# Performance work log

Measured on AMD Instinct MI355X. Metric: run time of the kernel, lower is better.

Reference implementation:

```python
import jax, jax.numpy as jnp
import numpy as np


def _mlp(x, W1, b1, W2, b2):
    # x: (B, M, T); torch MLPLayer: transpose(1,2) -> Linear -> Linear -> LeakyReLU -> transpose back
    h = jnp.einsum('bmt,hm->bht', x, W1) + b1[None, :, None]   # (B, H, T)
    y = jnp.einsum('bht,oh->bot', h, W2) + b2[None, :, None]   # (B, M, T)
    return jax.nn.leaky_relu(y, negative_slope=0.01)


def _calc_attn(q, k, v):
    # q: (B, M, Tq), k: (B, M, Tk), v: (B, M, Tk)
    Tq = q.shape[-1]
    qk = jnp.einsum('bmq,bmk->bqk', q, k)                       # (B, Tq, Tk)
    eye = jnp.eye(Tq, dtype=qk.dtype)                           # broadcasts: (Tq,Tq) or (1,1)
    logits = jnp.exp(qk - qk * eye / jnp.sqrt(jnp.asarray(Tq, qk.dtype)))
    scores = jax.nn.softmax(logits, axis=-1)
    return jnp.einsum('bqk,bmk->bmq', scores, v)                # (B, M, Tq)


def setup_inputs() -> dict:
    key = jax.random.key(0)
    B, M, T, H = 16, 128, 2048, 512
    ks = jax.random.split(key, 14)
    s = 0.02
    inp = {
        'pattern': jax.random.normal(ks[0], (B, M, T), jnp.float32),
        'value': jax.random.normal(ks[1], (B, M, T), jnp.float32),
        'kernel_size': 33,
    }
    names = ['q', 'k', 'o']
    for i, n in enumerate(names):
        inp['W%s1' % n] = jax.random.normal(ks[2 + 4 * i], (H, M), jnp.float32) * s
        inp['b%s1' % n] = jax.random.normal(ks[3 + 4 * i], (H,), jnp.float32) * s
        inp['W%s2' % n] = jax.random.normal(ks[4 + 4 * i], (M, H), jnp.float32) * s
        inp['b%s2' % n] = jax.random.normal(ks[5 + 4 * i], (M,), jnp.float32) * s
    return inp


def reference(pattern, value, kernel_size, Wq1, bq1, Wq2, bq2, Wk1, bk1, Wk2, bk2, Wo1, bo1, Wo2, bo2):
    query = _mlp(pattern, Wq1, bq1, Wq2, bq2)
    key = _mlp(pattern, Wk1, bk1, Wk2, bk2)
    # full (internal) attention
    attn_in = _calc_attn(query, key, value)                     # (B, M, T)
    rep_in = _mlp(attn_in, Wo1, bo1, Wo2, bo2)
    # windowed (external) attention
    T = query.shape[-1]
    cu = (kernel_size - 1) // 2
    q_w = query[..., T - 1 - cu : T - cu]                       # (B, M, 1)
    k_w = key[..., kernel_size - cu - 1 : T - cu - 2]           # (B, M, T-k-1)
    v_w = value[..., kernel_size : T - 1]                       # (B, M, T-k-1)
    attn_ex = _calc_attn(q_w, k_w, v_w)                         # (B, M, 1)
    rep_ex = _mlp(attn_ex, Wo1, bo1, Wo2, bo2)
    return jnp.concatenate([rep_in, rep_ex], axis=-1)           # (B, M, T+1)
```

## Files before the change

### kernel.cpp

```cpp
#include <hip/hip_runtime.h>
#include <hip/hip_bf16.h>
#include <math.h>

#define B_    16
#define M_    128
#define T_    2048
#define H_    512
#define TOUT_ 2049

typedef unsigned short u16;
typedef unsigned int   u32;
typedef __bf16 bf16x8 __attribute__((ext_vector_type(8)));
typedef float  f32x16 __attribute__((ext_vector_type(16)));
typedef float  f32x4  __attribute__((ext_vector_type(4)));
typedef u32    u32x4  __attribute__((ext_vector_type(4)));
typedef u32    u32x2  __attribute__((ext_vector_type(2)));

#define A_OFF     0
#define C_OFF     16384
#define MEAN_OFF  16896
#define AQKBF_OFF 19200
#define AOBF_OFF  35584
#define QT_OFF    43776
#define KT_OFF    (43776 + 2097152)
#define VB_OFF    (43776 + 2 * 2097152)

static __device__ __forceinline__ u16 f2bf(float f) {
  u32 u = __float_as_uint(f);
  u = (u + 0x7FFFu + ((u >> 16) & 1u)) >> 16;
  return (u16)u;
}
static __device__ __forceinline__ u32 pk2(float lo, float hi) {
  __hip_bfloat162 h = __float22bfloat162_rn(float2{lo, hi});
  u32 r;
  __builtin_memcpy(&r, &h, 4);
  return r;
}
static __device__ __forceinline__ bf16x8 ldfrag(const u16* p) {
  return __builtin_bit_cast(bf16x8, *(const u32x4*)p);
}

__global__ __launch_bounds__(128) void fuse_weights_all(
    const float* __restrict__ W1q, const float* __restrict__ b1q,
    const float* __restrict__ W2q, const float* __restrict__ b2q,
    const float* __restrict__ W1k, const float* __restrict__ b1k,
    const float* __restrict__ W2k, const float* __restrict__ b2k,
    const float* __restrict__ W1o, const float* __restrict__ b1o,
    const float* __restrict__ W2o, const float* __restrict__ b2o,
    float* __restrict__ A, float* __restrict__ c,
    u16* __restrict__ Aqk_bf, u16* __restrict__ Ao_bf) {
  __shared__ float w2row[H_];
  int which = blockIdx.x >> 7;
  int o = blockIdx.x & 127;
  const float* W1 = which == 0 ? W1q : which == 1 ? W1k : W1o;
  const float* b1 = which == 0 ? b1q : which == 1 ? b1k : b1o;
  const float* W2 = which == 0 ? W2q : which == 1 ? W2k : W2o;
  const float* b2 = which == 0 ? b2q : which == 1 ? b2k : b2o;
  int m = threadIdx.x;
  for (int h = m; h < H_; h += 128) w2row[h] = W2[o * H_ + h];
  __syncthreads();
  float acc = 0.f;
#pragma unroll 8
  for (int h = 0; h < H_; ++h) acc = fmaf(w2row[h], W1[h * M_ + m], acc);
  u16 ab = f2bf(acc);
  if (which == 0)      Aqk_bf[o * 128 + m] = ab;
  else if (which == 1) Aqk_bf[(128 + o) * 128 + m] = ab;
  else               { Ao_bf[o * 128 + m] = ab; A[o * M_ + m] = acc; }
  if (m < 64) {
    float cc = 0.f;
    for (int h = m; h < H_; h += 64) cc = fmaf(w2row[h], b1[h], cc);
#pragma unroll
    for (int off = 32; off > 0; off >>= 1) cc += __shfl_down(cc, off, 64);
    if (m == 0) c[which * 128 + o] = cc + b2[o];
  }
}

#define XS 68

__global__ __launch_bounds__(256) void prep_kernel(
    const float* __restrict__ pattern, const u16* __restrict__ Aqk_bf,
    const float* __restrict__ cqk, u16* __restrict__ qT, u16* __restrict__ kT,
    const float* __restrict__ value, u16* __restrict__ vb,
    float* __restrict__ meanv) {
  __shared__ alignas(16) float xsf[128 * XS];
  int bx = blockIdx.x;
  int tid = threadIdx.x;

  if (bx >= 512) {
    int bm = bx - 512;
    float* red = xsf;
    const float* row = value + (size_t)bm * T_;
    int i0 = tid * 8;
    float4 a = *(const float4*)(row + i0);
    float4 bq = *(const float4*)(row + i0 + 4);
    u32x4 o = {pk2(a.x, a.y), pk2(a.z, a.w), pk2(bq.x, bq.y), pk2(bq.z, bq.w)};
    *(u32x4*)&vb[(size_t)bm * T_ + i0] = o;
    float vals[8] = {a.x, a.y, a.z, a.w, bq.x, bq.y, bq.z, bq.w};
    float s = 0.f;
#pragma unroll
    for (int j = 0; j < 8; ++j) {
      int idx = i0 + j;
      if (idx >= 33 && idx < T_ - 1) s += vals[j];
    }
    red[tid] = s;
    __syncthreads();
    for (int st = 128; st > 0; st >>= 1) {
      if (tid < st) red[tid] += red[tid + st];
      __syncthreads();
    }
    if (tid == 0) meanv[bm] = red[0] * (1.f / 2014.f);
    return;
  }

  int b = bx >> 5;
  int t0 = (bx & 31) * 64;
  int lane = tid & 63;
  int wv = tid >> 6;
  int l31 = lane & 31;
  int lh8 = (lane >> 5) * 8;

  bf16x8 afr[2][8];
#pragma unroll
  for (int i = 0; i < 2; ++i) {
    const u16* ap = Aqk_bf + ((2 * wv + i) * 32 + l31) * 128 + lh8;
#pragma unroll
    for (int s = 0; s < 8; ++s) afr[i][s] = ldfrag(ap + 16 * s);
  }

#pragma unroll
  for (int rep = 0; rep < 8; ++rep) {
    int m = rep * 16 + (tid >> 4);
    int tc = (tid & 15) * 4;
    float4 v = *(const float4*)&pattern[(size_t)(b * M_ + m) * T_ + t0 + tc];
    *(float4*)&xsf[m * XS + tc] = v;
  }
  __syncthreads();

  bf16x8 bfr[2][8];
#pragma unroll
  for (int tt = 0; tt < 2; ++tt) {
#pragma unroll
    for (int s = 0; s < 8; ++s) {
      float v0 = xsf[(s * 16 + lh8 + 0) * XS + tt * 32 + l31];
      float v1 = xsf[(s * 16 + lh8 + 1) * XS + tt * 32 + l31];
      float v2 = xsf[(s * 16 + lh8 + 2) * XS + tt * 32 + l31];
      float v3 = xsf[(s * 16 + lh8 + 3) * XS + tt * 32 + l31];
      float v4 = xsf[(s * 16 + lh8 + 4) * XS + tt * 32 + l31];
      float v5 = xsf[(s * 16 + lh8 + 5) * XS + tt * 32 + l31];
      float v6 = xsf[(s * 16 + lh8 + 6) * XS + tt * 32 + l31];
      float v7 = xsf[(s * 16 + lh8 + 7) * XS + tt * 32 + l31];
      u32x4 p = {pk2(v0, v1), pk2(v2, v3), pk2(v4, v5), pk2(v6, v7)};
      bfr[tt][s] = __builtin_bit_cast(bf16x8, p);
    }
  }
  __syncthreads();

  u16* obuf = (u16*)xsf;
#pragma unroll
  for (int tt = 0; tt < 2; ++tt) {
#pragma unroll
    for (int i = 0; i < 2; ++i) {
      f32x16 acc;
#pragma unroll
      for (int r = 0; r < 16; ++r) acc[r] = 0.f;
#pragma unroll
      for (int s = 0; s < 8; ++s)
        acc = __builtin_amdgcn_mfma_f32_32x32x16_bf16(afr[i][s], bfr[tt][s], acc, 0, 0, 0);
      int ot = 2 * wv + i;
      int t = tt * 32 + l31;
#pragma unroll
      for (int r = 0; r < 16; ++r) {
        int orow = (r & 3) + 8 * (r >> 2) + 4 * (lane >> 5);
        float v = acc[r] + cqk[ot * 32 + orow];
        v = v > 0.f ? v : 0.01f * v;
        obuf[t * 258 + ot * 32 + orow] = f2bf(v);
      }
    }
  }
  __syncthreads();

  const u32* ob32 = (const u32*)obuf;
#pragma unroll
  for (int g = 0; g < 8; ++g) {
    int G = wv * 8 + g;
    int mat = G >> 4;
    int t = (G & 15) * 4 + (lane >> 4);
    int og2 = lane & 15;
    int wbase = t * 129 + mat * 64 + og2 * 4;
    u32x4 vv = {ob32[wbase], ob32[wbase + 1], ob32[wbase + 2], ob32[wbase + 3]};
    u32* dst = (u32*)((mat ? kT : qT) + ((size_t)(b * T_ + t0 + t)) * 128) + og2 * 4;
    *(u32x4*)dst = vv;
  }
}

#define QSTR 136
#define VSTR 72
#define NKT  (T_ / 64)

__global__ __launch_bounds__(512, 2) void attn_mfma_kernel(
    const u16* __restrict__ qT, const u16* __restrict__ kT,
    const u16* __restrict__ vB, const u16* __restrict__ Ao_bf,
    const float* __restrict__ co, const float* __restrict__ Aofp,
    const float* __restrict__ meanv, float* __restrict__ out) {
  extern __shared__ u16 smem[];
  u16* qsw = smem;
  u16* ks0 = smem + 128 * QSTR;
  u16* ks1 = ks0 + 64 * QSTR;
  u16* vs0 = ks1 + 64 * QSTR;
  u16* vs1 = vs0 + 128 * VSTR;
  float* dls  = (float*)(vs1 + 128 * VSTR);
  float* pbuf = (float*)ks0;

  int b = blockIdx.y;
  int q0 = blockIdx.x * 128;
  int tid = threadIdx.x;
  int lane = tid & 63;
  int wv = tid >> 6;
  int l31 = lane & 31;
  int h = lane >> 5;
  int lh8 = h * 8;
  int qt = wv & 3;
  int kh = wv >> 2;

  {
    const u16* gq = qT + (size_t)(b * T_ + q0) * 128;
#pragma unroll
    for (int it = 0; it < 4; ++it) {
      int r = it * 32 + (tid >> 4);
      int cm = (tid & 15) * 8;
      *(u32x4*)&qsw[r * QSTR + cm] = *(const u32x4*)&gq[r * 128 + cm];
    }
  }

  const u16* gkb = kT + (size_t)b * T_ * 128;
  const u16* gvb = vB + (size_t)b * M_ * T_;
  int kr = tid >> 4, kc = (tid & 15) * 8;
  int vr = tid >> 3, vc = (tid & 7) * 8;

  u32x4 kreg[2], vreg[2];
#pragma unroll
  for (int it = 0; it < 2; ++it) {
    kreg[it] = *(const u32x4*)&gkb[(size_t)(it * 32 + kr) * 128 + kc];
    vreg[it] = *(const u32x4*)&gvb[(size_t)(it * 64 + vr) * T_ + vc];
  }

  __syncthreads();

  bf16x8 qfrag[8];
  {
    const u16* qrow = &qsw[(qt * 32 + l31) * QSTR + lh8];
#pragma unroll
    for (int s = 0; s < 8; ++s) qfrag[s] = ldfrag(qrow + s * 16);
  }

#pragma unroll
  for (int it = 0; it < 2; ++it) {
    *(u32x4*)&ks0[(it * 32 + kr) * QSTR + kc] = kreg[it];
    *(u32x4*)&vs0[(it * 64 + vr) * VSTR + vc] = vreg[it];
  }
#pragma unroll
  for (int it = 0; it < 2; ++it) {
    kreg[it] = *(const u32x4*)&gkb[(size_t)(64 + it * 32 + kr) * 128 + kc];
    vreg[it] = *(const u32x4*)&gvb[(size_t)(it * 64 + vr) * T_ + 64 + vc];
  }

  f32x16 pacc[4];
  float den = 0.f;
#pragma unroll
  for (int i = 0; i < 16; ++i) {
    pacc[0][i] = 0.f; pacc[1][i] = 0.f; pacc[2][i] = 0.f; pacc[3][i] = 0.f;
  }

  for (int kt = 0; kt < NKT; ++kt) {
    int k0 = kt * 64;
    u16* kcur = (kt & 1) ? ks1 : ks0;
    u16* knxt = (kt & 1) ? ks0 : ks1;
    u16* vcur = (kt & 1) ? vs1 : vs0;
    u16* vnxt = (kt & 1) ? vs0 : vs1;
    __syncthreads();

    if (kt < NKT - 1) {
#pragma unroll
      for (int it = 0; it < 2; ++it) {
        *(u32x4*)&knxt[(it * 32 + kr) * QSTR + kc] = kreg[it];
        *(u32x4*)&vnxt[(it * 64 + vr) * VSTR + vc] = vreg[it];
      }
      int kn = (kt + 2 < NKT) ? (kt + 2) * 64 : (NKT - 1) * 64;
#pragma unroll
      for (int it = 0; it < 2; ++it) {
        kreg[it] = *(const u32x4*)&gkb[(size_t)(kn + it * 32 + kr) * 128 + kc];
        vreg[it] = *(const u32x4*)&gvb[(size_t)(it * 64 + vr) * T_ + kn + vc];
      }
    }

    f32x16 sacc;
#pragma unroll
    for (int i = 0; i < 16; ++i) sacc[i] = 0.f;
    {
      const u16* krow = &kcur[(kh * 32 + l31) * QSTR + lh8];
#pragma unroll
      for (int s = 0; s < 8; ++s) {
        bf16x8 kf = ldfrag(krow + s * 16);
        sacc = __builtin_amdgcn_mfma_f32_32x32x16_bf16(kf, qfrag[s], sacc, 0, 0, 0);
      }
    }

    if (k0 + kh * 32 == q0 + qt * 32) {
#pragma unroll
      for (int r = 0; r < 16; ++r) {
        int row = (r & 3) + 8 * (r >> 2) + 4 * h;
        if (row == l31) sacc[r] *= 0.97790291f;
      }
    }

    float w[16];
#pragma unroll
    for (int r = 0; r < 16; ++r) w[r] = __expf(__expf(sacc[r]));
#pragma unroll
    for (int r = 0; r < 16; ++r) den += w[r];
    u32 p00 = pk2(w[0], w[1]),  p01 = pk2(w[2], w[3]);
    u32 p10 = pk2(w[4], w[5]),  p11 = pk2(w[6], w[7]);
    u32 p20 = pk2(w[8], w[9]),  p21 = pk2(w[10], w[11]);
    u32 p30 = pk2(w[12], w[13]), p31 = pk2(w[14], w[15]);
    u32 e0 = __shfl_xor(h ? p00 : p10, 32, 64);
    u32 e1 = __shfl_xor(h ? p01 : p11, 32, 64);
    u32 e2 = __shfl_xor(h ? p20 : p30, 32, 64);
    u32 e3 = __shfl_xor(h ? p21 : p31, 32, 64);
    u32x4 f0 = h ? u32x4{e0, e1, p10, p11} : u32x4{p00, p01, e0, e1};
    u32x4 f1 = h ? u32x4{e2, e3, p30, p31} : u32x4{p20, p21, e2, e3};
    bf16x8 bw0 = __builtin_bit_cast(bf16x8, f0);
    bf16x8 bw1 = __builtin_bit_cast(bf16x8, f1);

#pragma unroll
    for (int mt = 0; mt < 4; ++mt) {
      const u16* vrow = &vcur[(mt * 32 + l31) * VSTR + kh * 32 + lh8];
      bf16x8 vf0 = ldfrag(vrow);
      bf16x8 vf1 = ldfrag(vrow + 16);
      pacc[mt] = __builtin_amdgcn_mfma_f32_32x32x16_bf16(vf0, bw0, pacc[mt], 0, 0, 0);
      pacc[mt] = __builtin_amdgcn_mfma_f32_32x32x16_bf16(vf1, bw1, pacc[mt], 0, 0, 0);
    }
  }

  float dq = den + __shfl_xor(den, 32, 64);

  __syncthreads();

  if (kh == 1) {
#pragma unroll
    for (int mt = 0; mt < 4; ++mt) {
      float* pb = &pbuf[((size_t)(qt * 4 + mt) * 64 + lane) * 16];
#pragma unroll
      for (int g = 0; g < 4; ++g) {
        f32x4 v = {pacc[mt][4 * g], pacc[mt][4 * g + 1],
                   pacc[mt][4 * g + 2], pacc[mt][4 * g + 3]};
        *(f32x4*)(pb + 4 * g) = v;
      }
    }
    if (lane < 32) dls[qt * 32 + lane] = dq;
  }
  __syncthreads();

  if (kh == 0) {
    float rden = 1.f / (dq + dls[qt * 32 + l31]);
#pragma unroll
    for (int mt = 0; mt < 4; ++mt) {
      const float* pb = &pbuf[((size_t)(qt * 4 + mt) * 64 + lane) * 16];
#pragma unroll
      for (int g = 0; g < 4; ++g) {
        f32x4 t = *(const f32x4*)(pb + 4 * g);
        float v0 = (pacc[mt][4 * g + 0] + t[0]) * rden;
        float v1 = (pacc[mt][4 * g + 1] + t[1]) * rden;
        float v2 = (pacc[mt][4 * g + 2] + t[2]) * rden;
        float v3 = (pacc[mt][4 * g + 3] + t[3]) * rden;
        int m0 = mt * 32 + 8 * g + 4 * h;
        u32x2 wp = {pk2(v0, v1), pk2(v2, v3)};
        *(u32x2*)&qsw[(qt * 32 + l31) * QSTR + m0] = wp;
      }
    }
  }
  __syncthreads();

  bf16x8 aofr[8];
  {
    const u16* ap = Ao_bf + ((wv & 3) * 32 + l31) * 128 + lh8;
#pragma unroll
    for (int s = 0; s < 8; ++s) aofr[s] = ldfrag(ap + 16 * s);
  }
#pragma unroll
  for (int j = 0; j < 2; ++j) {
    int qt2 = kh * 2 + j;
    bf16x8 pfr[8];
    const u16* pp = &qsw[(qt2 * 32 + l31) * QSTR + lh8];
#pragma unroll
    for (int s = 0; s < 8; ++s) pfr[s] = ldfrag(pp + 16 * s);
    f32x16 oacc;
#pragma unroll
    for (int r = 0; r < 16; ++r) oacc[r] = 0.f;
#pragma unroll
    for (int s = 0; s < 8; ++s)
      oacc = __builtin_amdgcn_mfma_f32_32x32x16_bf16(aofr[s], pfr[s], oacc, 0, 0, 0);
#pragma unroll
    for (int r = 0; r < 16; ++r) {
      int orow = (wv & 3) * 32 + (r & 3) + 8 * (r >> 2) + 4 * h;
      float v = oacc[r] + co[orow];
      v = v > 0.f ? v : 0.01f * v;
      out[((size_t)(b * M_ + orow)) * TOUT_ + q0 + qt2 * 32 + l31] = v;
    }
  }

  if (blockIdx.x == 0 && tid < 128) {
    float acc = co[tid];
    const float* mv = meanv + b * 128;
    for (int m = 0; m < 128; ++m) acc = fmaf(Aofp[tid * 128 + m], mv[m], acc);
    acc = acc > 0.f ? acc : 0.01f * acc;
    out[((size_t)(b * M_ + tid)) * TOUT_ + 2048] = acc;
  }
}

extern "C" void kernel_launch(void* const* d_in, const int* in_sizes, int n_in,
                              void* d_out, int out_size, void* d_ws, size_t ws_size,
                              hipStream_t stream) {
  (void)in_sizes; (void)n_in; (void)out_size; (void)ws_size;
  const float* pattern = (const float*)d_in[0];
  const float* value   = (const float*)d_in[1];
  const float* Wq1 = (const float*)d_in[3];
  const float* bq1 = (const float*)d_in[4];
  const float* Wq2 = (const float*)d_in[5];
  const float* bq2 = (const float*)d_in[6];
  const float* Wk1 = (const float*)d_in[7];
  const float* bk1 = (const float*)d_in[8];
  const float* Wk2 = (const float*)d_in[9];
  const float* bk2 = (const float*)d_in[10];
  const float* Wo1 = (const float*)d_in[11];
  const float* bo1 = (const float*)d_in[12];
  const float* Wo2 = (const float*)d_in[13];
  const float* bo2 = (const float*)d_in[14];

  float* ws     = (float*)d_ws;
  float* A      = ws + A_OFF;
  float* c      = ws + C_OFF;
  float* meanv  = ws + MEAN_OFF;
  u16*   Aqk_bf = (u16*)(ws + AQKBF_OFF);
  u16*   Ao_bf  = (u16*)(ws + AOBF_OFF);
  u16*   qT     = (u16*)(ws + QT_OFF);
  u16*   kT     = (u16*)(ws + KT_OFF);
  u16*   vB     = (u16*)(ws + VB_OFF);
  float* out    = (float*)d_out;

  fuse_weights_all<<<384, 128, 0, stream>>>(
      Wq1, bq1, Wq2, bq2, Wk1, bk1, Wk2, bk2, Wo1, bo1, Wo2, bo2,
      A, c, Aqk_bf, Ao_bf);

  prep_kernel<<<512 + B_ * M_, 256, 0, stream>>>(
      pattern, Aqk_bf, c, qT, kT, value, vB, meanv);

  size_t lds_bytes = (size_t)(128 * QSTR + 2 * 64 * QSTR + 2 * 128 * VSTR) * 2
                   + 128 * 4;
  attn_mfma_kernel<<<dim3(T_ / 128, B_), 512, lds_bytes, stream>>>(
      qT, kT, vB, Ao_bf, c + 256, A, meanv, out);
}
```

Baseline: 191.1 us.

## Halve attention query tile, fold log2e into q, use exp2 and setprio

Shrinks the attention block from 128 to 64 query rows with 256 threads. Q fragments now load straight from global memory instead of through LDS, and the grid doubles for better CU coverage. The double exponential is rewritten as nested exp2: log2e is pre-scaled into q in prep and a constant offset goes into the accumulator init, with the diagonal term corrected to match. The K/V prefetch is moved after the QK MFMAs, MFMA sections are wrapped in s_setprio, and the denominator sum becomes a tree. In exchange, K/V tiles are reloaded by twice as many blocks, and scaling q before bf16 rounding changes numerics slightly.

```diff
diff --git a/kernel.cpp b/kernel.cpp
--- a/kernel.cpp
+++ b/kernel.cpp
@@ -38,6 +38,13 @@
 }
 static __device__ __forceinline__ bf16x8 ldfrag(const u16* p) {
   return __builtin_bit_cast(bf16x8, *(const u32x4*)p);
+}
+static __device__ __forceinline__ float ex2(float x) {
+#if __has_builtin(__builtin_amdgcn_exp2f)
+  return __builtin_amdgcn_exp2f(x);
+#else
+  return exp2f(x);
+#endif
 }
 
 __global__ __launch_bounds__(128) void fuse_weights_all(
@@ -168,12 +175,13 @@
         acc = __builtin_amdgcn_mfma_f32_32x32x16_bf16(afr[i][s], bfr[tt][s], acc, 0, 0, 0);
       int ot = 2 * wv + i;
       int t = tt * 32 + l31;
+      float sc = (ot < 4) ? 1.44269504f : 1.0f;
 #pragma unroll
       for (int r = 0; r < 16; ++r) {
         int orow = (r & 3) + 8 * (r >> 2) + 4 * (lane >> 5);
         float v = acc[r] + cqk[ot * 32 + orow];
         v = v > 0.f ? v : 0.01f * v;
-        obuf[t * 258 + ot * 32 + orow] = f2bf(v);
+        obuf[t * 258 + ot * 32 + orow] = f2bf(v * sc);
       }
     }
   }
@@ -196,72 +204,61 @@
 #define QSTR 136
 #define VSTR 72
 #define NKT  (T_ / 64)
-
-__global__ __launch_bounds__(512, 2) void attn_mfma_kernel(
+#define CINIT 0.52876637f
+
+__global__ __launch_bounds__(256, 2) void attn_mfma_kernel(
     const u16* __restrict__ qT, const u16* __restrict__ kT,
     const u16* __restrict__ vB, const u16* __restrict__ Ao_bf,
     const float* __restrict__ co, const float* __restrict__ Aofp,
     const float* __restrict__ meanv, float* __restrict__ out) {
   extern __shared__ u16 smem[];
-  u16* qsw = smem;
-  u16* ks0 = smem + 128 * QSTR;
+  u16* ks0 = smem;
   u16* ks1 = ks0 + 64 * QSTR;
   u16* vs0 = ks1 + 64 * QSTR;
   u16* vs1 = vs0 + 128 * VSTR;
   float* dls  = (float*)(vs1 + 128 * VSTR);
   float* pbuf = (float*)ks0;
+  u16*   ptbuf = vs0;
 
   int b = blockIdx.y;
-  int q0 = blockIdx.x * 128;
+  int q0 = blockIdx.x * 64;
   int tid = threadIdx.x;
   int lane = tid & 63;
   int wv = tid >> 6;
   int l31 = lane & 31;
   int h = lane >> 5;
   int lh8 = h * 8;
-  int qt = wv & 3;
-  int kh = wv >> 2;
-
-  {
-    const u16* gq = qT + (size_t)(b * T_ + q0) * 128;
-#pragma unroll
-    for (int it = 0; it < 4; ++it) {
-      int r = it * 32 + (tid >> 4);
-      int cm = (tid & 15) * 8;
-      *(u32x4*)&qsw[r * QSTR + cm] = *(const u32x4*)&gq[r * 128 + cm];
-    }
-  }
+  int qt = wv & 1;
+  int kh = wv >> 1;
 
   const u16* gkb = kT + (size_t)b * T_ * 128;
   const u16* gvb = vB + (size_t)b * M_ * T_;
   int kr = tid >> 4, kc = (tid & 15) * 8;
   int vr = tid >> 3, vc = (tid & 7) * 8;
 
-  u32x4 kreg[2], vreg[2];
-#pragma unroll
-  for (int it = 0; it < 2; ++it) {
-    kreg[it] = *(const u32x4*)&gkb[(size_t)(it * 32 + kr) * 128 + kc];
-    vreg[it] = *(const u32x4*)&gvb[(size_t)(it * 64 + vr) * T_ + vc];
-  }
-
-  __syncthreads();
+  u32x4 kreg[4], vreg[4];
+#pragma unroll
+  for (int it = 0; it < 4; ++it) {
+    kreg[it] = *(const u32x4*)&gkb[(size_t)(it * 16 + kr) * 128 + kc];
+    vreg[it] = *(const u32x4*)&gvb[(size_t)(it * 32 + vr) * T_ + vc];
+  }
 
   bf16x8 qfrag[8];
   {
-    const u16* qrow = &qsw[(qt * 32 + l31) * QSTR + lh8];
+    const u16* qrow = qT + (size_t)(b * T_ + q0 + qt * 32 + l31) * 128 + lh8;
 #pragma unroll
     for (int s = 0; s < 8; ++s) qfrag[s] = ldfrag(qrow + s * 16);
   }
 
 #pragma unroll
-  for (int it = 0; it < 2; ++it) {
-    *(u32x4*)&ks0[(it * 32 + kr) * QSTR + kc] = kreg[it];
-    *(u32x4*)&vs0[(it * 64 + vr) * VSTR + vc] = vreg[it];
-  }
-#pragma unroll
-  for (int it = 0; it < 2; ++it) {
-    kreg[it] = *(const u32x4*)&gkb[(size_t)(64 + it * 32 + kr) * 128 + kc];
-    vreg[it] = *(const u32x4*)&gvb[(size_t)(it * 64 + vr) * T_ + 64 + vc];
+  for (int it = 0; it < 4; ++it) {
+    *(u32x4*)&ks0[(it * 16 + kr) * QSTR + kc] = kreg[it];
+    *(u32x4*)&vs0[(it * 32 + vr) * VSTR + vc] = vreg[it];
+  }
+#pragma unroll
+  for (int it = 0; it < 4; ++it) {
+    kreg[it] = *(const u32x4*)&gkb[(size_t)(64 + it * 16 + kr) * 128 + kc];
+    vreg[it] = *(const u32x4*)&gvb[(size_t)(it * 32 + vr) * T_ + 64 + vc];
   }
 
   f32x16 pacc[4];
@@ -279,45 +276,52 @@
     u16* vnxt = (kt & 1) ? vs0 : vs1;
     __syncthreads();
 
-    if (kt < NKT - 1) {
-#pragma unroll
-      for (int it = 0; it < 2; ++it) {
-        *(u32x4*)&knxt[(it * 32 + kr) * QSTR + kc] = kreg[it];
-        *(u32x4*)&vnxt[(it * 64 + vr) * VSTR + vc] = vreg[it];
-      }
-      int kn = (kt + 2 < NKT) ? (kt + 2) * 64 : (NKT - 1) * 64;
-#pragma unroll
-      for (int it = 0; it < 2; ++it) {
-        kreg[it] = *(const u32x4*)&gkb[(size_t)(kn + it * 32 + kr) * 128 + kc];
-        vreg[it] = *(const u32x4*)&gvb[(size_t)(it * 64 + vr) * T_ + kn + vc];
-      }
-    }
-
     f32x16 sacc;
 #pragma unroll
-    for (int i = 0; i < 16; ++i) sacc[i] = 0.f;
+    for (int i = 0; i < 16; ++i) sacc[i] = CINIT;
     {
       const u16* krow = &kcur[(kh * 32 + l31) * QSTR + lh8];
+      __builtin_amdgcn_s_setprio(1);
 #pragma unroll
       for (int s = 0; s < 8; ++s) {
         bf16x8 kf = ldfrag(krow + s * 16);
         sacc = __builtin_amdgcn_mfma_f32_32x32x16_bf16(kf, qfrag[s], sacc, 0, 0, 0);
       }
+      __builtin_amdgcn_s_setprio(0);
+    }
+
+    if (kt < NKT - 1) {
+#pragma unroll
+      for (int it = 0; it < 4; ++it) {
+        *(u32x4*)&knxt[(it * 16 + kr) * QSTR + kc] = kreg[it];
+        *(u32x4*)&vnxt[(it * 32 + vr) * VSTR + vc] = vreg[it];
+      }
+      int kn = (kt + 2 < NKT) ? (kt + 2) * 64 : (NKT - 1) * 64;
+#pragma unroll
+      for (int it = 0; it < 4; ++it) {
+        kreg[it] = *(const u32x4*)&gkb[(size_t)(kn + it * 16 + kr) * 128 + kc];
+        vreg[it] = *(const u32x4*)&gvb[(size_t)(it * 32 + vr) * T_ + kn + vc];
+      }
     }
 
     if (k0 + kh * 32 == q0 + qt * 32) {
 #pragma unroll
       for (int r = 0; r < 16; ++r) {
         int row = (r & 3) + 8 * (r >> 2) + 4 * h;
-        if (row == l31) sacc[r] *= 0.97790291f;
+        if (row == l31) sacc[r] = fmaf(sacc[r], 0.97790291f, 0.01168420f);
       }
     }
 
     float w[16];
 #pragma unroll
-    for (int r = 0; r < 16; ++r) w[r] = __expf(__expf(sacc[r]));
-#pragma unroll
-    for (int r = 0; r < 16; ++r) den += w[r];
+    for (int r = 0; r < 16; ++r) w[r] = ex2(ex2(sacc[r]));
+    {
+      float d0 = (w[0] + w[1]) + (w[2] + w[3]);
+      float d1 = (w[4] + w[5]) + (w[6] + w[7]);
+      float d2 = (w[8] + w[9]) + (w[10] + w[11]);
+      float d3 = (w[12] + w[13]) + (w[14] + w[15]);
+      den += (d0 + d1) + (d2 + d3);
+    }
     u32 p00 = pk2(w[0], w[1]),  p01 = pk2(w[2], w[3]);
     u32 p10 = pk2(w[4], w[5]),  p11 = pk2(w[6], w[7]);
     u32 p20 = pk2(w[8], w[9]),  p21 = pk2(w[10], w[11]);
@@ -331,6 +335,7 @@
     bf16x8 bw0 = __builtin_bit_cast(bf16x8, f0);
     bf16x8 bw1 = __builtin_bit_cast(bf16x8, f1);
 
+    __builtin_amdgcn_s_setprio(1);
 #pragma unroll
     for (int mt = 0; mt < 4; ++mt) {
       const u16* vrow = &vcur[(mt * 32 + l31) * VSTR + kh * 32 + lh8];
@@ -339,6 +344,7 @@
       pacc[mt] = __builtin_amdgcn_mfma_f32_32x32x16_bf16(vf0, bw0, pacc[mt], 0, 0, 0);
       pacc[mt] = __builtin_amdgcn_mfma_f32_32x32x16_bf16(vf1, bw1, pacc[mt], 0, 0, 0);
     }
+    __builtin_amdgcn_s_setprio(0);
   }
 
   float dq = den + __shfl_xor(den, 32, 64);
@@ -374,7 +380,7 @@
         float v3 = (pacc[mt][4 * g + 3] + t[3]) * rden;
         int m0 = mt * 32 + 8 * g + 4 * h;
         u32x2 wp = {pk2(v0, v1), pk2(v2, v3)};
-        *(u32x2*)&qsw[(qt * 32 + l31) * QSTR + m0] = wp;
+        *(u32x2*)&ptbuf[(qt * 32 + l31) * QSTR + m0] = wp;
       }
     }
   }
@@ -382,15 +388,14 @@
 
   bf16x8 aofr[8];
   {
-    const u16* ap = Ao_bf + ((wv & 3) * 32 + l31) * 128 + lh8;
+    const u16* ap = Ao_bf + (wv * 32 + l31) * 128 + lh8;
 #pragma unroll
     for (int s = 0; s < 8; ++s) aofr[s] = ldfrag(ap + 16 * s);
   }
 #pragma unroll
   for (int j = 0; j < 2; ++j) {
-    int qt2 = kh * 2 + j;
     bf16x8 pfr[8];
-    const u16* pp = &qsw[(qt2 * 32 + l31) * QSTR + lh8];
+    const u16* pp = &ptbuf[(j * 32 + l31) * QSTR + lh8];
 #pragma unroll
     for (int s = 0; s < 8; ++s) pfr[s] = ldfrag(pp + 16 * s);
     f32x16 oacc;
@@ -401,10 +406,10 @@
       oacc = __builtin_amdgcn_mfma_f32_32x32x16_bf16(aofr[s], pfr[s], oacc, 0, 0, 0);
 #pragma unroll
     for (int r = 0; r < 16; ++r) {
-      int orow = (wv & 3) * 32 + (r & 3) + 8 * (r >> 2) + 4 * h;
+      int orow = wv * 32 + (r & 3) + 8 * (r >> 2) + 4 * h;
       float v = oacc[r] + co[orow];
       v = v > 0.f ? v : 0.01f * v;
-      out[((size_t)(b * M_ + orow)) * TOUT_ + q0 + qt2 * 32 + l31] = v;
+      out[((size_t)(b * M_ + orow)) * TOUT_ + q0 + j * 32 + l31] = v;
     }
   }
 
@@ -454,8 +459,7 @@
   prep_kernel<<<512 + B_ * M_, 256, 0, stream>>>(
       pattern, Aqk_bf, c, qT, kT, value, vB, meanv);
 
-  size_t lds_bytes = (size_t)(128 * QSTR + 2 * 64 * QSTR + 2 * 128 * VSTR) * 2
-                   + 128 * 4;
-  attn_mfma_kernel<<<dim3(T_ / 128, B_), 512, lds_bytes, stream>>>(
+  size_t lds_bytes = (size_t)(2 * 64 * QSTR + 2 * 128 * VSTR) * 2 + 64 * 4;
+  attn_mfma_kernel<<<dim3(T_ / 64, B_), 256, lds_bytes, stream>>>(
       qT, kT, vB, Ao_bf, c + 256, A, meanv, out);
 }
```

Result: slower. 196.9 us (+3.0%).
